# Optimization experiments

Hardware: AMD Instinct MI355X
Metric: run time of the kernel (lower is better)

The kernel has to match this reference:

```python
import jax, jax.numpy as jnp
from jax import lax
import numpy as np

H = 48; W = 48; C_IN = 256; A_PER = 3
M = A_PER * H * W            # 6912 anchors
IMG = 768.0                  # square image, clip bound for x and y
OBJ_THR = 0.3; IOU_THR = 0.7; TOP_K = 2000
NEG = -1e9                   # finite sentinel for masked scores


def _make_anchors():
    stride = IMG / H
    base = 2.0 * stride
    ratios = np.array([0.5, 1.0, 2.0])
    ws = base * np.sqrt(ratios)          # [3]
    hs = base / np.sqrt(ratios)
    cx = (np.arange(W) + 0.5) * stride
    cy = (np.arange(H) + 0.5) * stride
    cxg, cyg = np.meshgrid(cx, cy)       # [H, W]
    anc = np.stack([
        cxg[None] - ws[:, None, None] / 2,
        cyg[None] - hs[:, None, None] / 2,
        cxg[None] + ws[:, None, None] / 2,
        cyg[None] + hs[:, None, None] / 2,
    ], axis=-1)                           # [3, H, W, 4] matches (anchor, h, w) flatten order
    return jnp.asarray(anc.reshape(-1, 4), jnp.float32)


def setup_inputs() -> dict:
    key = jax.random.key(0)
    ks = jax.random.split(key, 4)
    x = jax.random.normal(ks[0], (1, C_IN, H, W), jnp.float32)
    conv_w = jax.random.normal(ks[1], (256, 256, 3, 3), jnp.float32) * 0.02
    conv_b = jnp.zeros((256,), jnp.float32)
    det_w = jax.random.normal(ks[2], (3, 256, 1, 1), jnp.float32) * 0.02
    det_b = jnp.zeros((3,), jnp.float32)
    reg_w = jax.random.normal(ks[3], (12, 256, 1, 1), jnp.float32) * 0.02
    reg_b = jnp.zeros((12,), jnp.float32)
    anchors = _make_anchors()
    return {"x": x, "conv_w": conv_w, "conv_b": conv_b, "det_w": det_w,
            "det_b": det_b, "reg_w": reg_w, "reg_b": reg_b, "anchors": anchors}


def reference(x, conv_w, conv_b, det_w, det_b, reg_w, reg_b, anchors):
    # ---- FPN 3x3 conv + RPN head (1x1 convs) ----
    inter = lax.conv_general_dilated(
        x, conv_w, (1, 1), 'SAME',
        dimension_numbers=('NCHW', 'OIHW', 'NCHW')) + conv_b[None, :, None, None]
    obj = jax.nn.sigmoid(jnp.einsum('nchw,oc->nohw', inter, det_w[:, :, 0, 0])
                         + det_b[None, :, None, None])          # [1,3,H,W]
    reg = (jnp.einsum('nchw,oc->nohw', inter, reg_w[:, :, 0, 0])
           + reg_b[None, :, None, None])                        # [1,12,H,W]

    scores = obj.reshape(-1)                                    # [M], (anchor,h,w) order
    deltas = reg.reshape(1, 4, A_PER, H, W).transpose(0, 2, 3, 4, 1).reshape(-1, 4)

    # ---- box decode (preserves the source's cx/cy quirk: cx = y1 + w/2, cy = x1 + h/2) ----
    x1, y1, x2, y2 = anchors[:, 0], anchors[:, 1], anchors[:, 2], anchors[:, 3]
    aw = x2 - x1; ah = y2 - y1
    acx = y1 + aw / 2; acy = x1 + ah / 2
    dx, dy, dw, dh = deltas[:, 0], deltas[:, 1], deltas[:, 2], deltas[:, 3]
    px = acx + dx * aw; py = acy + dy * ah
    pw = aw * jnp.exp(dw); ph = ah * jnp.exp(dh)
    boxes = jnp.stack([px - pw / 2, py - ph / 2, px + pw / 2, py + ph / 2], axis=-1)

    # ---- clip to image ----
    boxes = jnp.clip(boxes, 0.0, IMG)

    # ---- validity: degenerate filter (source's naming quirk) + objectness threshold ----
    hts = boxes[:, 2] - boxes[:, 0]
    wds = boxes[:, 3] - boxes[:, 1]
    valid = (hts > 0) & (wds > 0) & (scores > OBJ_THR)

    # ---- greedy NMS (jit-friendly: sort, pairwise IoU, sequential suppression) ----
    s = jnp.where(valid, scores, NEG)
    order = jnp.argsort(-s)
    b = boxes[order]; v = valid[order]; ss = s[order]
    area = (b[:, 2] - b[:, 0]) * (b[:, 3] - b[:, 1])             # [M]
    iw = jnp.clip(jnp.minimum(b[:, None, 2], b[None, :, 2])
                  - jnp.maximum(b[:, None, 0], b[None, :, 0]), 0.0)
    ih = jnp.clip(jnp.minimum(b[:, None, 3], b[None, :, 3])
                  - jnp.maximum(b[:, None, 1], b[None, :, 1]), 0.0)
    inter_a = iw * ih                                             # [M,M]
    iou = inter_a / jnp.maximum(area[:, None] + area[None, :] - inter_a, 1e-9)

    idx = jnp.arange(M)

    def body(suppressed, i):
        keep_i = v[i] & (~suppressed[i])
        sup = keep_i & (iou[i] > IOU_THR) & (idx > i)
        return suppressed | sup, keep_i

    _, keeps = lax.scan(body, jnp.zeros(M, bool), idx)            # keep mask (sorted order)

    # ---- top-k proposal selection (fixed K, padded with sentinels) ----
    out_s = jnp.where(keeps, ss, NEG)
    topv, topi = lax.top_k(out_s, TOP_K)
    vtop = keeps[topi]
    out_scores = jnp.where(vtop, topv, -1.0)                      # [TOP_K]
    out_boxes = jnp.where(vtop[:, None], b[topi], 0.0)            # [TOP_K, 4]
    return out_scores, out_boxes
```

## Files before the change

kernel.cpp:

```cpp
#include <hip/hip_runtime.h>
#include <cstdint>

#define NPX 2304
#define MM 6912
#define NW 108
#define TOPK 2000
#define NEGV -1000000000.0f
#define OBJ_THRF 0.3f
#define IOU_THRF 0.7f
#define IMGF 768.0f
#define KSPLIT 8

typedef unsigned long long u64;
typedef unsigned int u32;

__device__ __forceinline__ u64 shfl64(u64 v, int src) {
  int lo = __shfl((int)(v & 0xffffffffull), src, 64);
  int hi = __shfl((int)(v >> 32), src, 64);
  return ((u64)(u32)hi << 32) | (u32)lo;
}

__global__ __launch_bounds__(256) void k_wt(const float* __restrict__ cw,
                                            float* __restrict__ wt) {
  __shared__ float t[64][65];
  const int it0 = blockIdx.x * 64;
  const int oc0 = blockIdx.y * 64;
  const int tx = threadIdx.x & 63;
  const int ty = threadIdx.x >> 6;
#pragma unroll
  for (int k = 0; k < 16; ++k) {
    int oc = ty + k * 4;
    t[oc][tx] = cw[(oc0 + oc) * 2304 + it0 + tx];
  }
  __syncthreads();
#pragma unroll
  for (int k = 0; k < 16; ++k) {
    int it = ty + k * 4;
    wt[(it0 + it) * 256 + oc0 + tx] = t[tx][it];
  }
}

__global__ __launch_bounds__(256) void k_conv(const float* __restrict__ x,
                                              const float* __restrict__ wt,
                                              float* __restrict__ part) {
  __shared__ float xs[8 * 8 * 52];
  const int tid = threadIdx.x;
  const int px = blockIdx.x * 256 + tid;
  const int oc0 = blockIdx.y * 8;
  const int ks = blockIdx.z;
  const int row = px / 48, col = px % 48;
  const int r0 = (blockIdx.x * 256) / 48;
  const int rbase = row - r0;

  float acc[8];
#pragma unroll
  for (int k = 0; k < 8; ++k) acc[k] = 0.f;

  for (int icc = 0; icc < 4; ++icc) {
    const int ic0 = ks * 32 + icc * 8;
    for (int e = tid; e < 8 * 8 * 50; e += 256) {
      int ic = e / 400, rem = e % 400;
      int r = rem / 50, c = rem % 50 - 1;
      int gr = r0 - 1 + r;
      float v = 0.f;
      if (c >= 0 && c < 48 && gr >= 0 && gr < 48)
        v = x[(ic0 + ic) * NPX + gr * 48 + c];
      xs[(ic * 8 + r) * 52 + (c + 1)] = v;
    }
    __syncthreads();
    for (int ic = 0; ic < 8; ++ic) {
      float xv[9];
#pragma unroll
      for (int dr = 0; dr < 3; ++dr)
#pragma unroll
        for (int dc = 0; dc < 3; ++dc)
          xv[dr * 3 + dc] = xs[(ic * 8 + rbase + dr) * 52 + col + dc];
      const float* wrow = wt + (size_t)(ic0 + ic) * 9 * 256 + oc0;
#pragma unroll
      for (int t = 0; t < 9; ++t) {
        const float* wp = wrow + t * 256;
#pragma unroll
        for (int k = 0; k < 8; ++k) acc[k] += xv[t] * wp[k];
      }
    }
    __syncthreads();
  }
#pragma unroll
  for (int k = 0; k < 8; ++k)
    part[((size_t)ks * 256 + oc0 + k) * NPX + px] = acc[k];
}

__global__ __launch_bounds__(64) void k_dq(const float* __restrict__ part,
                                           const float* __restrict__ cb,
                                           const float* __restrict__ dw,
                                           const float* __restrict__ rw,
                                           float* __restrict__ qacc) {
  __shared__ float wl[64 * 16];
  const int tid = threadIdx.x;
  const int cq = blockIdx.y;
  const int px = blockIdx.x * 64 + tid;
  for (int e = tid; e < 960; e += 64) {
    int o = e % 15, ci = e / 15;
    int c = cq * 64 + ci;
    wl[ci * 16 + o] = (o < 3) ? dw[o * 256 + c] : rw[(o - 3) * 256 + c];
  }
  __syncthreads();
  float acc[15];
#pragma unroll
  for (int o = 0; o < 15; o++) acc[o] = 0.f;
#pragma unroll 4
  for (int ci = 0; ci < 64; ++ci) {
    int c = cq * 64 + ci;
    float v = cb[c];
#pragma unroll
    for (int kks = 0; kks < KSPLIT; ++kks)
      v += part[((size_t)kks * 256 + c) * NPX + px];
#pragma unroll
    for (int o = 0; o < 15; o++) acc[o] += v * wl[ci * 16 + o];
  }
#pragma unroll
  for (int o = 0; o < 15; o++)
    qacc[((size_t)cq * NPX + px) * 16 + o] = acc[o];
}

__global__ __launch_bounds__(64) void k_dfin(const float* __restrict__ qacc,
                                             const float* __restrict__ db,
                                             const float* __restrict__ rb,
                                             const float* __restrict__ anch,
                                             float* __restrict__ s,
                                             float4* __restrict__ boxes) {
  const int tid = threadIdx.x;
  const int p = blockIdx.x * 64 + tid;
  float a[15];
#pragma unroll
  for (int o = 0; o < 15; o++)
    a[o] = qacc[((size_t)0 * NPX + p) * 16 + o] +
           qacc[((size_t)1 * NPX + p) * 16 + o] +
           qacc[((size_t)2 * NPX + p) * 16 + o] +
           qacc[((size_t)3 * NPX + p) * 16 + o];
  const float4* an4 = (const float4*)anch;
#pragma unroll
  for (int aa = 0; aa < 3; ++aa) {
    int m = aa * NPX + p;
    float logit = a[aa] + db[aa];
    float score = 1.f / (1.f + expf(-logit));
    float dxv = a[3 + 0 + aa] + rb[0 + aa];
    float dyv = a[3 + 3 + aa] + rb[3 + aa];
    float dwv = a[3 + 6 + aa] + rb[6 + aa];
    float dhv = a[3 + 9 + aa] + rb[9 + aa];
    float4 an = an4[m];
    float aw = an.z - an.x;
    float ah = an.w - an.y;
    float acx = an.y + aw * 0.5f;
    float acy = an.x + ah * 0.5f;
    float pxc = acx + dxv * aw;
    float pyc = acy + dyv * ah;
    float pw = aw * expf(dwv);
    float ph = ah * expf(dhv);
    float b0 = pxc - pw * 0.5f, b1 = pyc - ph * 0.5f;
    float b2 = pxc + pw * 0.5f, b3 = pyc + ph * 0.5f;
    b0 = fminf(fmaxf(b0, 0.f), IMGF);
    b1 = fminf(fmaxf(b1, 0.f), IMGF);
    b2 = fminf(fmaxf(b2, 0.f), IMGF);
    b3 = fminf(fmaxf(b3, 0.f), IMGF);
    float hts = b2 - b0, wds = b3 - b1;
    bool valid = (hts > 0.f) && (wds > 0.f) && (score > OBJ_THRF);
    s[m] = valid ? score : NEGV;
    boxes[m] = make_float4(b0, b1, b2, b3);
  }
}

__global__ __launch_bounds__(256) void k_sortA(const float* __restrict__ s,
                                               u64* __restrict__ keys) {
  __shared__ u64 lds[1024];
  const int tid = threadIdx.x;
  const int b = blockIdx.x;
  for (int v = tid; v < 1024; v += 256) {
    int i = b * 1024 + v;
    u64 p;
    if (i < MM) {
      u32 u = __float_as_uint(s[i]);
      u = u ^ (u32)(((int)u >> 31) | 0x80000000);
      p = ((u64)(~u) << 32) | (u32)i;
    } else {
      p = ~0ull;
    }
    lds[v] = p;
  }
  for (u32 kk = 2; kk <= 1024; kk <<= 1) {
    for (u32 j = kk >> 1; j > 0; j >>= 1) {
      __syncthreads();
#pragma unroll 2
      for (int t = tid; t < 512; t += 256) {
        int i = ((t & ~(j - 1)) << 1) | (t & (j - 1));
        int l = i | j;
        bool up = ((i & kk) == 0);
        u64 a = lds[i], c = lds[l];
        u64 mn = a < c ? a : c;
        u64 mx = a < c ? c : a;
        lds[i] = up ? mn : mx;
        lds[l] = up ? mx : mn;
      }
    }
  }
  __syncthreads();
  for (int v = tid; v < 1024; v += 256) keys[b * 1024 + v] = lds[v];
}

__global__ __launch_bounds__(256) void k_merge(const u64* __restrict__ in,
                                               u64* __restrict__ outk, int L, int fin,
                                               const float* __restrict__ s,
                                               const float4* __restrict__ boxes,
                                               float* __restrict__ ssc,
                                               float4* __restrict__ sboxes) {
  const int i = blockIdx.x * 256 + threadIdx.x;
  const int pair = i / (2 * L);
  const int r = i - pair * 2 * L;
  const u64* A = in + (size_t)pair * 2 * L;
  const u64* B = A + L;
  int lo = (r > L) ? (r - L) : 0;
  int hi = (r < L) ? r : L;
  while (lo < hi) {
    int mid = (lo + hi) >> 1;
    if (A[mid] < B[r - 1 - mid]) lo = mid + 1; else hi = mid;
  }
  int a = lo, bi = r - lo;
  u64 av = (a < L) ? A[a] : ~0ull;
  u64 bv = (bi < L) ? B[bi] : ~0ull;
  u64 o = (av < bv) ? av : bv;
  outk[i] = o;
  if (fin && i < MM) {
    int idx = (int)(u32)o;
    ssc[i] = s[idx];
    sboxes[i] = boxes[idx];
  }
}

__global__ __launch_bounds__(256) void k_zero(u64* __restrict__ nz) {
  int i = blockIdx.x * 256 + threadIdx.x;
  if (i < MM * 2) nz[i] = 0;
}

__global__ __launch_bounds__(256) void k_mask(const float4* __restrict__ sboxes,
                                              u64* __restrict__ mask_t,
                                              u64* __restrict__ nz) {
  __shared__ float4 rb_[64];
  const int rt = blockIdx.x;
  const int w = blockIdx.y * 4 + (threadIdx.x >> 6);
  const int lane = threadIdx.x & 63;
  if (threadIdx.x < 64) rb_[threadIdx.x] = sboxes[rt * 64 + threadIdx.x];
  __syncthreads();
  if (w < rt) return;
  float4 c = sboxes[w * 64 + lane];
  float areaC = (c.z - c.x) * (c.w - c.y);
  u64 myw = 0;
  for (int r = 0; r < 64; ++r) {
    float4 b = rb_[r];
    float iw = fmaxf(fminf(b.z, c.z) - fmaxf(b.x, c.x), 0.f);
    float ih = fmaxf(fminf(b.w, c.w) - fmaxf(b.y, c.y), 0.f);
    float inter = iw * ih;
    float areaB = (b.z - b.x) * (b.w - b.y);
    float un = fmaxf(areaB + areaC - inter, 1e-9f);
    bool bit = (inter / un) > IOU_THRF;
    u64 bal = __ballot(bit);
    if (lane == r) myw = bal;
  }
  mask_t[(size_t)w * MM + rt * 64 + lane] = myw;
  if (myw) atomicOr(&nz[(rt * 64 + lane) * 2 + (w >> 6)], 1ull << (w & 63));
}

__global__ __launch_bounds__(256) void k_scan(const u64* __restrict__ mask_t,
                                              const u64* __restrict__ nz,
                                              const float* __restrict__ ssc,
                                              const float4* __restrict__ sboxes,
                                              float* __restrict__ out) {
  __shared__ u64 remv[NW];
  __shared__ u64 keepw[NW];
  __shared__ int blist[64];
  __shared__ int nkS;
  __shared__ int kcntS;
  __shared__ int pref[NW];
  const int tid = threadIdx.x;
  if (tid < NW) { remv[tid] = 0; keepw[tid] = 0; }
  if (tid == 0) kcntS = 0;
  __syncthreads();

  for (int c = 0; c < NW; ++c) {
    if (tid < 64) {
      const int lane = tid;
      u64 dg = mask_t[(size_t)c * MM + c * 64 + lane];
      float sv = ssc[c * 64 + lane];
      u64 vb = __ballot(sv > OBJ_THRF);
      u64 w0 = remv[c];
      u64 cand = vb & ~w0;
      u64 above = (lane < 63) ? ~((2ull << lane) - 1ull) : 0ull;
      bool inC = ((cand >> lane) & 1ull) != 0;
      u64 conf = __ballot(inC && ((dg & above & cand) != 0ull));
      u64 kb;
      if (conf == 0ull) {
        kb = cand;
      } else {
        u64 w = w0;
        kb = 0;
        u64 rem = cand;
        while (rem) {
          int b = __ffsll(rem) - 1;
          kb |= (1ull << b);
          w |= shfl64(dg, b);
          rem = vb & ~w;
        }
      }
      int below = __popcll(kb & ((1ull << lane) - 1ull));
      if ((kb >> lane) & 1ull) blist[below] = lane;
      if (lane == 0) {
        keepw[c] = kb;
        nkS = __popcll(kb);
        kcntS += __popcll(kb);
      }
    }
    __syncthreads();
    int nk = nkS;
    if (tid < nk) {
      int row = c * 64 + blist[tid];
      u64 nz0 = nz[row * 2], nz1 = nz[row * 2 + 1];
      if (c < 64) {
        nz0 &= (c < 63) ? ~((2ull << c) - 1ull) : 0ull;
      } else {
        nz0 = 0;
        int cc = c - 64;
        nz1 &= ~((2ull << cc) - 1ull);
      }
      while (nz0) {
        int wv = __ffsll(nz0) - 1; nz0 &= nz0 - 1;
        atomicOr(&remv[wv], mask_t[(size_t)wv * MM + row]);
      }
      while (nz1) {
        int wv = __ffsll(nz1) - 1; nz1 &= nz1 - 1;
        atomicOr(&remv[wv + 64], mask_t[(size_t)(wv + 64) * MM + row]);
      }
    }
    __syncthreads();
    if (kcntS >= TOPK) break;
  }

  if (tid == 0) {
    int run = 0;
    for (int cc = 0; cc < NW; ++cc) { pref[cc] = run; run += __popcll(keepw[cc]); }
  }
  __syncthreads();
  for (int e = tid; e < TOPK * 5; e += 256) out[e] = (e < TOPK) ? -1.0f : 0.0f;
  __syncthreads();
  float4* ob = (float4*)(out + TOPK);
  for (int i = tid; i < MM; i += 256) {
    int cc = i >> 6, b = i & 63;
    u64 kb = keepw[cc];
    if ((kb >> b) & 1ull) {
      int rank = pref[cc] + __popcll(kb & ((1ull << b) - 1ull));
      if (rank < TOPK) {
        out[rank] = ssc[i];
        ob[rank] = sboxes[i];
      }
    }
  }
}

extern "C" void kernel_launch(void* const* d_in, const int* in_sizes, int n_in,
                              void* d_out, int out_size, void* d_ws, size_t ws_size,
                              hipStream_t stream) {
  const float* x  = (const float*)d_in[0];
  const float* cw = (const float*)d_in[1];
  const float* cb = (const float*)d_in[2];
  const float* dw = (const float*)d_in[3];
  const float* db = (const float*)d_in[4];
  const float* rw = (const float*)d_in[5];
  const float* rb = (const float*)d_in[6];
  const float* an = (const float*)d_in[7];
  char* ws = (char*)d_ws;
  float*  part   = (float*)(ws);
  u64*    keysA  = (u64*)(ws);
  u64*    keysB  = (u64*)(ws + 65536);
  u64*    mask   = (u64*)(ws);
  u64*    nz     = (u64*)(ws + 5971968);
  float*  wt     = (float*)(ws + 18874368);
  float*  qacc   = (float*)(ws + 18874368);
  float*  s      = (float*)(ws + 21233664);
  float4* boxes  = (float4*)(ws + 21261312);
  float*  ssc    = (float*)(ws + 21371904);
  float4* sboxes = (float4*)(ws + 21399552);
  float* out = (float*)d_out;

  hipLaunchKernelGGL(k_wt, dim3(36, 4), dim3(256), 0, stream, cw, wt);
  hipLaunchKernelGGL(k_conv, dim3(9, 32, KSPLIT), dim3(256), 0, stream, x, wt, part);
  hipLaunchKernelGGL(k_dq, dim3(36, 4), dim3(64), 0, stream, part, cb, dw, rw, qacc);
  hipLaunchKernelGGL(k_dfin, dim3(36), dim3(64), 0, stream, qacc, db, rb, an, s, boxes);
  hipLaunchKernelGGL(k_zero, dim3(54), dim3(256), 0, stream, nz);
  hipLaunchKernelGGL(k_sortA, dim3(8), dim3(256), 0, stream, s, keysA);
  hipLaunchKernelGGL(k_merge, dim3(32), dim3(256), 0, stream, keysA, keysB, 1024, 0, s, boxes, ssc, sboxes);
  hipLaunchKernelGGL(k_merge, dim3(32), dim3(256), 0, stream, keysB, keysA, 2048, 0, s, boxes, ssc, sboxes);
  hipLaunchKernelGGL(k_merge, dim3(32), dim3(256), 0, stream, keysA, keysB, 4096, 1, s, boxes, ssc, sboxes);
  hipLaunchKernelGGL(k_mask, dim3(108, 27), dim3(256), 0, stream, sboxes, mask, nz);
  hipLaunchKernelGGL(k_scan, dim3(1), dim3(256), 0, stream, mask, nz, ssc, sboxes, out);
}
```

Baseline: 282.6 us.

## Fuse head, decode, sort and merges into one cooperative kernel; retile conv

Removes the separate weight-transpose kernel. The conv now stages each block's weight slice and a 16-row input tile in LDS, and each thread computes 3 adjacent pixels to reuse input values across outputs. The 1x1 head, box decode, zeroing, block bitonic sort and three merge passes are fused into a single 8-block cooperative kernel that uses grid syncs, cutting the number of launches. This trades launch overhead for grid-wide barriers and lower parallelism in the head stage (8 blocks × 16 waves).

```diff
diff --git a/kernel.cpp b/kernel.cpp
--- a/kernel.cpp
+++ b/kernel.cpp
@@ -1,5 +1,8 @@
 #include <hip/hip_runtime.h>
+#include <hip/hip_cooperative_groups.h>
 #include <cstdint>
+
+namespace cg = cooperative_groups;
 
 #define NPX 2304
 #define MM 6912
@@ -20,200 +23,83 @@
   return ((u64)(u32)hi << 32) | (u32)lo;
 }
 
-__global__ __launch_bounds__(256) void k_wt(const float* __restrict__ cw,
-                                            float* __restrict__ wt) {
-  __shared__ float t[64][65];
-  const int it0 = blockIdx.x * 64;
-  const int oc0 = blockIdx.y * 64;
-  const int tx = threadIdx.x & 63;
-  const int ty = threadIdx.x >> 6;
-#pragma unroll
-  for (int k = 0; k < 16; ++k) {
-    int oc = ty + k * 4;
-    t[oc][tx] = cw[(oc0 + oc) * 2304 + it0 + tx];
-  }
-  __syncthreads();
-#pragma unroll
-  for (int k = 0; k < 16; ++k) {
-    int it = ty + k * 4;
-    wt[(it0 + it) * 256 + oc0 + tx] = t[tx][it];
-  }
-}
-
 __global__ __launch_bounds__(256) void k_conv(const float* __restrict__ x,
-                                              const float* __restrict__ wt,
+                                              const float* __restrict__ cw,
                                               float* __restrict__ part) {
-  __shared__ float xs[8 * 8 * 52];
+  __shared__ float xs[8 * 18 * 52];
+  __shared__ float wsh[32 * 9 * 8];
   const int tid = threadIdx.x;
-  const int px = blockIdx.x * 256 + tid;
+  const int ks = blockIdx.z;
   const int oc0 = blockIdx.y * 8;
-  const int ks = blockIdx.z;
-  const int row = px / 48, col = px % 48;
-  const int r0 = (blockIdx.x * 256) / 48;
-  const int rbase = row - r0;
-
-  float acc[8];
-#pragma unroll
-  for (int k = 0; k < 8; ++k) acc[k] = 0.f;
+  const int lr = tid >> 4;
+  const int c0 = (tid & 15) * 3;
+  const int br0 = blockIdx.x * 16;
+  const int grow = br0 + lr;
+
+  for (int e = tid; e < 2304; e += 256) {
+    int k = e / 288, r = e - k * 288;
+    wsh[r * 8 + k] = cw[(size_t)(oc0 + k) * 2304 + ks * 288 + r];
+  }
+
+  float acc[3][8];
+#pragma unroll
+  for (int p = 0; p < 3; ++p)
+#pragma unroll
+    for (int k = 0; k < 8; ++k) acc[p][k] = 0.f;
 
   for (int icc = 0; icc < 4; ++icc) {
-    const int ic0 = ks * 32 + icc * 8;
-    for (int e = tid; e < 8 * 8 * 50; e += 256) {
-      int ic = e / 400, rem = e % 400;
-      int r = rem / 50, c = rem % 50 - 1;
-      int gr = r0 - 1 + r;
+    const int icg = ks * 32 + icc * 8;
+    __syncthreads();
+    for (int e = tid; e < 8 * 18 * 50; e += 256) {
+      int ic = e / 900, rem = e - ic * 900;
+      int r = rem / 50, cc = rem - r * 50 - 1;
+      int gr = br0 - 1 + r;
       float v = 0.f;
-      if (c >= 0 && c < 48 && gr >= 0 && gr < 48)
-        v = x[(ic0 + ic) * NPX + gr * 48 + c];
-      xs[(ic * 8 + r) * 52 + (c + 1)] = v;
+      if (cc >= 0 && cc < 48 && gr >= 0 && gr < 48)
+        v = x[(size_t)(icg + ic) * NPX + gr * 48 + cc];
+      xs[(ic * 18 + r) * 52 + cc + 1] = v;
     }
     __syncthreads();
+#pragma unroll 2
     for (int ic = 0; ic < 8; ++ic) {
-      float xv[9];
+      float xr[15];
 #pragma unroll
       for (int dr = 0; dr < 3; ++dr)
 #pragma unroll
-        for (int dc = 0; dc < 3; ++dc)
-          xv[dr * 3 + dc] = xs[(ic * 8 + rbase + dr) * 52 + col + dc];
-      const float* wrow = wt + (size_t)(ic0 + ic) * 9 * 256 + oc0;
+        for (int j = 0; j < 5; ++j)
+          xr[dr * 5 + j] = xs[(ic * 18 + lr + dr) * 52 + c0 + j];
+      const int rb0 = (icc * 8 + ic) * 9;
 #pragma unroll
       for (int t = 0; t < 9; ++t) {
-        const float* wp = wrow + t * 256;
-#pragma unroll
-        for (int k = 0; k < 8; ++k) acc[k] += xv[t] * wp[k];
-      }
-    }
-    __syncthreads();
-  }
+        const int dr = t / 3, dc = t % 3;
+        const float4 wa = *(const float4*)&wsh[(rb0 + t) * 8];
+        const float4 wb = *(const float4*)&wsh[(rb0 + t) * 8 + 4];
+#pragma unroll
+        for (int p = 0; p < 3; ++p) {
+          const float xv = xr[dr * 5 + p + dc];
+          acc[p][0] += xv * wa.x;  acc[p][1] += xv * wa.y;
+          acc[p][2] += xv * wa.z;  acc[p][3] += xv * wa.w;
+          acc[p][4] += xv * wb.x;  acc[p][5] += xv * wb.y;
+          acc[p][6] += xv * wb.z;  acc[p][7] += xv * wb.w;
+        }
+      }
+    }
+  }
+  const int pxb = grow * 48 + c0;
 #pragma unroll
   for (int k = 0; k < 8; ++k)
-    part[((size_t)ks * 256 + oc0 + k) * NPX + px] = acc[k];
-}
-
-__global__ __launch_bounds__(64) void k_dq(const float* __restrict__ part,
-                                           const float* __restrict__ cb,
-                                           const float* __restrict__ dw,
-                                           const float* __restrict__ rw,
-                                           float* __restrict__ qacc) {
-  __shared__ float wl[64 * 16];
-  const int tid = threadIdx.x;
-  const int cq = blockIdx.y;
-  const int px = blockIdx.x * 64 + tid;
-  for (int e = tid; e < 960; e += 64) {
-    int o = e % 15, ci = e / 15;
-    int c = cq * 64 + ci;
-    wl[ci * 16 + o] = (o < 3) ? dw[o * 256 + c] : rw[(o - 3) * 256 + c];
-  }
-  __syncthreads();
-  float acc[15];
-#pragma unroll
-  for (int o = 0; o < 15; o++) acc[o] = 0.f;
-#pragma unroll 4
-  for (int ci = 0; ci < 64; ++ci) {
-    int c = cq * 64 + ci;
-    float v = cb[c];
-#pragma unroll
-    for (int kks = 0; kks < KSPLIT; ++kks)
-      v += part[((size_t)kks * 256 + c) * NPX + px];
-#pragma unroll
-    for (int o = 0; o < 15; o++) acc[o] += v * wl[ci * 16 + o];
-  }
-#pragma unroll
-  for (int o = 0; o < 15; o++)
-    qacc[((size_t)cq * NPX + px) * 16 + o] = acc[o];
-}
-
-__global__ __launch_bounds__(64) void k_dfin(const float* __restrict__ qacc,
-                                             const float* __restrict__ db,
-                                             const float* __restrict__ rb,
-                                             const float* __restrict__ anch,
-                                             float* __restrict__ s,
-                                             float4* __restrict__ boxes) {
-  const int tid = threadIdx.x;
-  const int p = blockIdx.x * 64 + tid;
-  float a[15];
-#pragma unroll
-  for (int o = 0; o < 15; o++)
-    a[o] = qacc[((size_t)0 * NPX + p) * 16 + o] +
-           qacc[((size_t)1 * NPX + p) * 16 + o] +
-           qacc[((size_t)2 * NPX + p) * 16 + o] +
-           qacc[((size_t)3 * NPX + p) * 16 + o];
-  const float4* an4 = (const float4*)anch;
-#pragma unroll
-  for (int aa = 0; aa < 3; ++aa) {
-    int m = aa * NPX + p;
-    float logit = a[aa] + db[aa];
-    float score = 1.f / (1.f + expf(-logit));
-    float dxv = a[3 + 0 + aa] + rb[0 + aa];
-    float dyv = a[3 + 3 + aa] + rb[3 + aa];
-    float dwv = a[3 + 6 + aa] + rb[6 + aa];
-    float dhv = a[3 + 9 + aa] + rb[9 + aa];
-    float4 an = an4[m];
-    float aw = an.z - an.x;
-    float ah = an.w - an.y;
-    float acx = an.y + aw * 0.5f;
-    float acy = an.x + ah * 0.5f;
-    float pxc = acx + dxv * aw;
-    float pyc = acy + dyv * ah;
-    float pw = aw * expf(dwv);
-    float ph = ah * expf(dhv);
-    float b0 = pxc - pw * 0.5f, b1 = pyc - ph * 0.5f;
-    float b2 = pxc + pw * 0.5f, b3 = pyc + ph * 0.5f;
-    b0 = fminf(fmaxf(b0, 0.f), IMGF);
-    b1 = fminf(fmaxf(b1, 0.f), IMGF);
-    b2 = fminf(fmaxf(b2, 0.f), IMGF);
-    b3 = fminf(fmaxf(b3, 0.f), IMGF);
-    float hts = b2 - b0, wds = b3 - b1;
-    bool valid = (hts > 0.f) && (wds > 0.f) && (score > OBJ_THRF);
-    s[m] = valid ? score : NEGV;
-    boxes[m] = make_float4(b0, b1, b2, b3);
-  }
-}
-
-__global__ __launch_bounds__(256) void k_sortA(const float* __restrict__ s,
-                                               u64* __restrict__ keys) {
-  __shared__ u64 lds[1024];
-  const int tid = threadIdx.x;
-  const int b = blockIdx.x;
-  for (int v = tid; v < 1024; v += 256) {
-    int i = b * 1024 + v;
-    u64 p;
-    if (i < MM) {
-      u32 u = __float_as_uint(s[i]);
-      u = u ^ (u32)(((int)u >> 31) | 0x80000000);
-      p = ((u64)(~u) << 32) | (u32)i;
-    } else {
-      p = ~0ull;
-    }
-    lds[v] = p;
-  }
-  for (u32 kk = 2; kk <= 1024; kk <<= 1) {
-    for (u32 j = kk >> 1; j > 0; j >>= 1) {
-      __syncthreads();
-#pragma unroll 2
-      for (int t = tid; t < 512; t += 256) {
-        int i = ((t & ~(j - 1)) << 1) | (t & (j - 1));
-        int l = i | j;
-        bool up = ((i & kk) == 0);
-        u64 a = lds[i], c = lds[l];
-        u64 mn = a < c ? a : c;
-        u64 mx = a < c ? c : a;
-        lds[i] = up ? mn : mx;
-        lds[l] = up ? mx : mn;
-      }
-    }
-  }
-  __syncthreads();
-  for (int v = tid; v < 1024; v += 256) keys[b * 1024 + v] = lds[v];
-}
-
-__global__ __launch_bounds__(256) void k_merge(const u64* __restrict__ in,
-                                               u64* __restrict__ outk, int L, int fin,
-                                               const float* __restrict__ s,
-                                               const float4* __restrict__ boxes,
-                                               float* __restrict__ ssc,
-                                               float4* __restrict__ sboxes) {
-  const int i = blockIdx.x * 256 + threadIdx.x;
+#pragma unroll
+    for (int p = 0; p < 3; ++p)
+      part[((size_t)ks * 256 + oc0 + k) * NPX + pxb + p] = acc[p][k];
+}
+
+__device__ __forceinline__ void merge_step(const u64* __restrict__ in,
+                                           u64* __restrict__ outk, int L, int i,
+                                           int fin,
+                                           const float* __restrict__ s,
+                                           const float4* __restrict__ boxes,
+                                           float* __restrict__ ssc,
+                                           float4* __restrict__ sboxes) {
   const int pair = i / (2 * L);
   const int r = i - pair * 2 * L;
   const u64* A = in + (size_t)pair * 2 * L;
@@ -236,9 +122,130 @@
   }
 }
 
-__global__ __launch_bounds__(256) void k_zero(u64* __restrict__ nz) {
-  int i = blockIdx.x * 256 + threadIdx.x;
-  if (i < MM * 2) nz[i] = 0;
+__global__ __launch_bounds__(1024) void k_tail(
+    const float* __restrict__ part, const float* __restrict__ cb,
+    const float* __restrict__ dw, const float* __restrict__ db,
+    const float* __restrict__ rw, const float* __restrict__ rb,
+    const float* __restrict__ anch,
+    float* __restrict__ qacc, float* __restrict__ s, float4* __restrict__ boxes,
+    u64* __restrict__ keysA, u64* __restrict__ keysB,
+    float* __restrict__ ssc, float4* __restrict__ sboxes,
+    u64* __restrict__ nz) {
+  cg::grid_group grid = cg::this_grid();
+  __shared__ float wl[256 * 16];
+  __shared__ u64 lds[1024];
+  const int tid = threadIdx.x;
+  const int bid = blockIdx.x;
+  const int gtid = bid * 1024 + tid;
+
+  for (int e = tid; e < 3840; e += 1024) {
+    int o = e % 15, c = e / 15;
+    wl[c * 16 + o] = (o < 3) ? dw[o * 256 + c] : rw[(o - 3) * 256 + c];
+  }
+  __syncthreads();
+
+  const int lane = tid & 63;
+  for (int task = bid * 16 + (tid >> 6); task < 144; task += 128) {
+    const int pxblk = task >> 2, cq = task & 3;
+    const int px = pxblk * 64 + lane;
+    float acc[15];
+#pragma unroll
+    for (int o = 0; o < 15; o++) acc[o] = 0.f;
+#pragma unroll 4
+    for (int ci = 0; ci < 64; ++ci) {
+      int c = cq * 64 + ci;
+      float v = cb[c];
+#pragma unroll
+      for (int kks = 0; kks < KSPLIT; ++kks)
+        v += part[((size_t)kks * 256 + c) * NPX + px];
+#pragma unroll
+      for (int o = 0; o < 15; o++) acc[o] += v * wl[c * 16 + o];
+    }
+#pragma unroll
+    for (int o = 0; o < 15; o++)
+      qacc[((size_t)cq * NPX + px) * 16 + o] = acc[o];
+  }
+  grid.sync();
+
+  for (int i = gtid; i < MM * 2; i += 8192) nz[i] = 0;
+  if (gtid < NPX) {
+    const int p = gtid;
+    float a[15];
+#pragma unroll
+    for (int o = 0; o < 15; o++)
+      a[o] = qacc[((size_t)0 * NPX + p) * 16 + o] +
+             qacc[((size_t)1 * NPX + p) * 16 + o] +
+             qacc[((size_t)2 * NPX + p) * 16 + o] +
+             qacc[((size_t)3 * NPX + p) * 16 + o];
+    const float4* an4 = (const float4*)anch;
+#pragma unroll
+    for (int aa = 0; aa < 3; ++aa) {
+      int m = aa * NPX + p;
+      float logit = a[aa] + db[aa];
+      float score = 1.f / (1.f + expf(-logit));
+      float dxv = a[3 + 0 + aa] + rb[0 + aa];
+      float dyv = a[3 + 3 + aa] + rb[3 + aa];
+      float dwv = a[3 + 6 + aa] + rb[6 + aa];
+      float dhv = a[3 + 9 + aa] + rb[9 + aa];
+      float4 an = an4[m];
+      float aw = an.z - an.x;
+      float ah = an.w - an.y;
+      float acx = an.y + aw * 0.5f;
+      float acy = an.x + ah * 0.5f;
+      float pxc = acx + dxv * aw;
+      float pyc = acy + dyv * ah;
+      float pw = aw * expf(dwv);
+      float ph = ah * expf(dhv);
+      float b0 = pxc - pw * 0.5f, b1 = pyc - ph * 0.5f;
+      float b2 = pxc + pw * 0.5f, b3 = pyc + ph * 0.5f;
+      b0 = fminf(fmaxf(b0, 0.f), IMGF);
+      b1 = fminf(fmaxf(b1, 0.f), IMGF);
+      b2 = fminf(fmaxf(b2, 0.f), IMGF);
+      b3 = fminf(fmaxf(b3, 0.f), IMGF);
+      float hts = b2 - b0, wds = b3 - b1;
+      bool valid = (hts > 0.f) && (wds > 0.f) && (score > OBJ_THRF);
+      s[m] = valid ? score : NEGV;
+      boxes[m] = make_float4(b0, b1, b2, b3);
+    }
+  }
+  grid.sync();
+
+  {
+    int i = bid * 1024 + tid;
+    u64 p;
+    if (i < MM) {
+      u32 u = __float_as_uint(s[i]);
+      u = u ^ (u32)(((int)u >> 31) | 0x80000000);
+      p = ((u64)(~u) << 32) | (u32)i;
+    } else {
+      p = ~0ull;
+    }
+    lds[tid] = p;
+    for (u32 kk = 2; kk <= 1024; kk <<= 1) {
+      for (u32 j = kk >> 1; j > 0; j >>= 1) {
+        __syncthreads();
+        if (tid < 512) {
+          int ii = ((tid & ~(j - 1)) << 1) | (tid & (j - 1));
+          int l = ii | j;
+          bool up = ((ii & kk) == 0);
+          u64 a = lds[ii], c = lds[l];
+          u64 mn = a < c ? a : c;
+          u64 mx = a < c ? c : a;
+          lds[ii] = up ? mn : mx;
+          lds[l] = up ? mx : mn;
+        }
+      }
+    }
+    __syncthreads();
+    keysA[bid * 1024 + tid] = lds[tid];
+  }
+  grid.sync();
+
+  merge_step(keysA, keysB, 1024, gtid, 0, s, boxes, ssc, sboxes);
+  grid.sync();
+  merge_step(keysB, keysA, 2048, gtid, 0, s, boxes, ssc, sboxes);
+  grid.sync();
+  merge_step(keysA, keysB, 4096, gtid, 1, s, boxes, ssc, sboxes);
 }
 
 __global__ __launch_bounds__(256) void k_mask(const float4* __restrict__ sboxes,
@@ -381,7 +388,6 @@
   u64*    keysB  = (u64*)(ws + 65536);
   u64*    mask   = (u64*)(ws);
   u64*    nz     = (u64*)(ws + 5971968);
-  float*  wt     = (float*)(ws + 18874368);
   float*  qacc   = (float*)(ws + 18874368);
   float*  s      = (float*)(ws + 21233664);
   float4* boxes  = (float4*)(ws + 21261312);
@@ -389,15 +395,15 @@
   float4* sboxes = (float4*)(ws + 21399552);
   float* out = (float*)d_out;
 
-  hipLaunchKernelGGL(k_wt, dim3(36, 4), dim3(256), 0, stream, cw, wt);
-  hipLaunchKernelGGL(k_conv, dim3(9, 32, KSPLIT), dim3(256), 0, stream, x, wt, part);
-  hipLaunchKernelGGL(k_dq, dim3(36, 4), dim3(64), 0, stream, part, cb, dw, rw, qacc);
-  hipLaunchKernelGGL(k_dfin, dim3(36), dim3(64), 0, stream, qacc, db, rb, an, s, boxes);
-  hipLaunchKernelGGL(k_zero, dim3(54), dim3(256), 0, stream, nz);
-  hipLaunchKernelGGL(k_sortA, dim3(8), dim3(256), 0, stream, s, keysA);
-  hipLaunchKernelGGL(k_merge, dim3(32), dim3(256), 0, stream, keysA, keysB, 1024, 0, s, boxes, ssc, sboxes);
-  hipLaunchKernelGGL(k_merge, dim3(32), dim3(256), 0, stream, keysB, keysA, 2048, 0, s, boxes, ssc, sboxes);
-  hipLaunchKernelGGL(k_merge, dim3(32), dim3(256), 0, stream, keysA, keysB, 4096, 1, s, boxes, ssc, sboxes);
+  hipLaunchKernelGGL(k_conv, dim3(3, 32, KSPLIT), dim3(256), 0, stream, x, cw, part);
+
+  void* targs[] = {(void*)&part, (void*)&cb, (void*)&dw, (void*)&db,
+                   (void*)&rw, (void*)&rb, (void*)&an,
+                   (void*)&qacc, (void*)&s, (void*)&boxes,
+                   (void*)&keysA, (void*)&keysB,
+                   (void*)&ssc, (void*)&sboxes, (void*)&nz};
+  hipLaunchCooperativeKernel((const void*)k_tail, dim3(8), dim3(1024), targs, 0, stream);
+
   hipLaunchKernelGGL(k_mask, dim3(108, 27), dim3(256), 0, stream, sboxes, mask, nz);
   hipLaunchKernelGGL(k_scan, dim3(1), dim3(256), 0, stream, mask, nz, ssc, sboxes, out);
 }
```

New measurement: 345.9 us. 1.22x slower.

## Widen conv output tile to 16 channels and prefetch input chunks in registers

Applied to the files above, without the earlier changes.

The 3x3 conv kernel now computes 16 output channels per thread instead of 8, which halves the grid's y-dimension and reuses each staged input tile across twice as many channels. Input staging moves to 16-channel chunks. The next chunk is prefetched from global memory into registers while the current one is written to shared memory, with explicit barriers and sched_barrier hints. This cuts redundant input loads and overlaps global latency with compute. In exchange it raises register pressure (25 staged values plus 16 accumulators), which may lower occupancy, and the grid shrinks to fewer blocks.

```diff
diff --git a/kernel.cpp b/kernel.cpp
--- a/kernel.cpp
+++ b/kernel.cpp
@@ -43,50 +43,78 @@
 __global__ __launch_bounds__(256) void k_conv(const float* __restrict__ x,
                                               const float* __restrict__ wt,
                                               float* __restrict__ part) {
-  __shared__ float xs[8 * 8 * 52];
+  __shared__ float xs[16 * 8 * 52];
   const int tid = threadIdx.x;
   const int px = blockIdx.x * 256 + tid;
-  const int oc0 = blockIdx.y * 8;
+  const int oc0 = blockIdx.y * 16;
   const int ks = blockIdx.z;
   const int row = px / 48, col = px % 48;
   const int r0 = (blockIdx.x * 256) / 48;
   const int rbase = row - r0;
 
-  float acc[8];
-#pragma unroll
-  for (int k = 0; k < 8; ++k) acc[k] = 0.f;
-
-  for (int icc = 0; icc < 4; ++icc) {
-    const int ic0 = ks * 32 + icc * 8;
-    for (int e = tid; e < 8 * 8 * 50; e += 256) {
+  float st[25];
+#pragma unroll
+  for (int k = 0; k < 25; ++k) {
+    int e = tid + k * 256;
+    int ic = e / 400, rem = e % 400;
+    int r = rem / 50, c = rem % 50 - 1;
+    int gr = r0 - 1 + r;
+    float v = 0.f;
+    if (c >= 0 && c < 48 && gr >= 0 && gr < 48)
+      v = x[(ks * 32 + ic) * NPX + gr * 48 + c];
+    st[k] = v;
+  }
+
+  float acc[16];
+#pragma unroll
+  for (int k = 0; k < 16; ++k) acc[k] = 0.f;
+
+  for (int icc = 0; icc < 2; ++icc) {
+    __builtin_amdgcn_sched_barrier(0);
+    __builtin_amdgcn_s_barrier();
+    __builtin_amdgcn_sched_barrier(0);
+#pragma unroll
+    for (int k = 0; k < 25; ++k) {
+      int e = tid + k * 256;
       int ic = e / 400, rem = e % 400;
-      int r = rem / 50, c = rem % 50 - 1;
-      int gr = r0 - 1 + r;
-      float v = 0.f;
-      if (c >= 0 && c < 48 && gr >= 0 && gr < 48)
-        v = x[(ic0 + ic) * NPX + gr * 48 + c];
-      xs[(ic * 8 + r) * 52 + (c + 1)] = v;
-    }
-    __syncthreads();
-    for (int ic = 0; ic < 8; ++ic) {
+      int r = rem / 50, c = rem % 50;
+      xs[(ic * 8 + r) * 52 + c] = st[k];
+    }
+    if (icc == 0) {
+#pragma unroll
+      for (int k = 0; k < 25; ++k) {
+        int e = tid + k * 256;
+        int ic = e / 400, rem = e % 400;
+        int r = rem / 50, c = rem % 50 - 1;
+        int gr = r0 - 1 + r;
+        float v = 0.f;
+        if (c >= 0 && c < 48 && gr >= 0 && gr < 48)
+          v = x[(ks * 32 + 16 + ic) * NPX + gr * 48 + c];
+        st[k] = v;
+      }
+    }
+    asm volatile("s_waitcnt lgkmcnt(0)" ::: "memory");
+    __builtin_amdgcn_s_barrier();
+    __builtin_amdgcn_sched_barrier(0);
+    const int icg0 = ks * 32 + icc * 16;
+    for (int ic = 0; ic < 16; ++ic) {
       float xv[9];
 #pragma unroll
       for (int dr = 0; dr < 3; ++dr)
 #pragma unroll
         for (int dc = 0; dc < 3; ++dc)
           xv[dr * 3 + dc] = xs[(ic * 8 + rbase + dr) * 52 + col + dc];
-      const float* wrow = wt + (size_t)(ic0 + ic) * 9 * 256 + oc0;
+      const float* wrow = wt + (size_t)(icg0 + ic) * 9 * 256 + oc0;
 #pragma unroll
       for (int t = 0; t < 9; ++t) {
         const float* wp = wrow + t * 256;
 #pragma unroll
-        for (int k = 0; k < 8; ++k) acc[k] += xv[t] * wp[k];
-      }
-    }
-    __syncthreads();
-  }
-#pragma unroll
-  for (int k = 0; k < 8; ++k)
+        for (int k = 0; k < 16; ++k) acc[k] += xv[t] * wp[k];
+      }
+    }
+  }
+#pragma unroll
+  for (int k = 0; k < 16; ++k)
     part[((size_t)ks * 256 + oc0 + k) * NPX + px] = acc[k];
 }
 
@@ -390,7 +418,7 @@
   float* out = (float*)d_out;
 
   hipLaunchKernelGGL(k_wt, dim3(36, 4), dim3(256), 0, stream, cw, wt);
-  hipLaunchKernelGGL(k_conv, dim3(9, 32, KSPLIT), dim3(256), 0, stream, x, wt, part);
+  hipLaunchKernelGGL(k_conv, dim3(9, 16, KSPLIT), dim3(256), 0, stream, x, wt, part);
   hipLaunchKernelGGL(k_dq, dim3(36, 4), dim3(64), 0, stream, part, cb, dw, rw, qacc);
   hipLaunchKernelGGL(k_dfin, dim3(36), dim3(64), 0, stream, qacc, db, rb, an, s, boxes);
   hipLaunchKernelGGL(k_zero, dim3(54), dim3(256), 0, stream, nz);
```

Result: slower. 323.8 us (+14.6%).
